# Kernel tuning notes

Hardware: AMD Instinct MI355X
Metric: run time of the kernel (lower is better)

## Reference

```python
import jax, jax.numpy as jnp
import numpy as np

EPS = 0.1        # entropic regularization
MAX_ITER = 50    # fixed iteration count (torch early-stops on host; we run all iters)
P = 1            # cost exponent
N_POINTS = 4096
D_FEAT = 2


def _cost_matrix(x, y):
    # x: [N, D], y: [M, D] -> C: [N, M], sum_d |x_i - y_j|^p
    return jnp.sum(jnp.abs(x[:, None, :] - y[None, :, :]) ** P, axis=-1)


def setup_inputs() -> dict:
    key = jax.random.key(0)
    k1, k2 = jax.random.split(key)
    x = jax.random.normal(k1, (N_POINTS, D_FEAT), dtype=jnp.float32)
    y = jax.random.normal(k2, (N_POINTS, D_FEAT), dtype=jnp.float32)
    return {"x": x, "y": y}


def reference(x, y):
    n, m = x.shape[0], y.shape[0]
    C = _cost_matrix(x, y)  # [N, M]
    log_mu = jnp.log(jnp.full((n,), 1.0 / n, dtype=x.dtype) + 1e-8)
    log_nu = jnp.log(jnp.full((m,), 1.0 / m, dtype=y.dtype) + 1e-8)

    def M(u, v):
        # modified cost: (-C + u_i + v_j) / eps
        return (-C + u[:, None] + v[None, :]) / EPS

    def step(carry, _):
        u, v = carry
        u = EPS * (log_mu - jax.scipy.special.logsumexp(M(u, v), axis=-1)) + u
        v = EPS * (log_nu - jax.scipy.special.logsumexp(M(u, v), axis=-2)) + v
        return (u, v), None

    u0 = jnp.zeros((n,), dtype=x.dtype)
    v0 = jnp.zeros((m,), dtype=y.dtype)
    (u, v), _ = jax.lax.scan(step, (u0, v0), None, length=MAX_ITER)

    pi = jnp.exp(M(u, v))                 # transport plan [N, M]
    cost = jnp.sum(pi * C)                # scalar (reduction='none', 2D input)
    return cost ** (1.0 / P), pi, C
```

## Files before the change

### kernel.cpp

```cpp
#include <hip/hip_runtime.h>


#define NPTS    4096
#define EPS_F   0.1f
#define S_L2E   14.426950408889634f
#define INV_SL  0.0693147180559945f
#define A_LOGMU (-0.8317725207f)
#define N_ITER  50
#define NLEAF   16
#define BSTRIDE 64
#define BAR_INTS ((NLEAF + 1 + NLEAF) * BSTRIDE)

typedef float f4u __attribute__((ext_vector_type(4), aligned(4)));

__device__ __forceinline__ float fexp2(float x) {
#if __has_builtin(__builtin_amdgcn_exp2f)
  return __builtin_amdgcn_exp2f(x);
#else
  float r;
  asm("v_exp_f32 %0, %1" : "=v"(r) : "v"(x));
  return r;
#endif
}

__device__ __forceinline__ float coh_load(const float* p) {
  return __hip_atomic_load(p, __ATOMIC_RELAXED, __HIP_MEMORY_SCOPE_AGENT);
}
__device__ __forceinline__ void coh_store(float* p, float x) {
  __hip_atomic_store(p, x, __ATOMIC_RELAXED, __HIP_MEMORY_SCOPE_AGENT);
}

__device__ __forceinline__ float wave_sum64(float x) {
#pragma unroll
  for (int off = 32; off > 0; off >>= 1) x += __shfl_xor(x, off, 64);
  return x;
}

__device__ __forceinline__ void grid_barrier(int* bar, int k, int arrpl) {
  __syncthreads();
  if (threadIdx.x == 0) {
    const int myleaf = blockIdx.x & (NLEAF - 1);
    const int old = __hip_atomic_fetch_add(bar + myleaf * BSTRIDE, 1,
                                           __ATOMIC_RELAXED,
                                           __HIP_MEMORY_SCOPE_AGENT);
    if (old == arrpl * k - 1)
      __hip_atomic_store(bar + (NLEAF + 1 + myleaf) * BSTRIDE, k,
                         __ATOMIC_RELAXED, __HIP_MEMORY_SCOPE_AGENT);
    for (;;) {
      int mn = k;
#pragma unroll
      for (int rr = 0; rr < NLEAF; ++rr) {
        const int f = __hip_atomic_load(bar + (NLEAF + 1 + rr) * BSTRIDE,
                                        __ATOMIC_RELAXED,
                                        __HIP_MEMORY_SCOPE_AGENT);
        mn = min(mn, f);
      }
      if (mn >= k) break;
      __builtin_amdgcn_s_sleep(1);
    }
  }
  __syncthreads();
}

#define SBLK  512
#define STPB  1024
#define SARR  (SBLK / NLEAF)
#define SCOLS 2048

__device__ __forceinline__ void stage_half(
    const float* __restrict__ part, const float* __restrict__ colp,
    float* __restrict__ sW, float* __restrict__ sC0, float* __restrict__ sC1,
    int tid, int colbase, bool zero) {
  const int c2 = tid * 2;
  const int g = colbase + c2;
  const float4 a = ((const float4*)colp)[g >> 1];
  float w0 = 0.f, w1 = 0.f;
  if (!zero) {
    const float p00 = coh_load(part + g), p01 = coh_load(part + g + 1);
    const float p10 = coh_load(part + NPTS + g);
    const float p11 = coh_load(part + NPTS + g + 1);
    w0 = (A_LOGMU - EPS_F * __logf(p00 + p10)) * S_L2E;
    w1 = (A_LOGMU - EPS_F * __logf(p01 + p11)) * S_L2E;
  }
  float2 W, C0, C1;
  W.x = w0;            W.y = w1;
  C0.x = a.x * S_L2E;  C0.y = a.z * S_L2E;
  C1.x = a.y * S_L2E;  C1.y = a.w * S_L2E;
  *(float2*)(sW + c2)  = W;
  *(float2*)(sC0 + c2) = C0;
  *(float2*)(sC1 + c2) = C1;
  __syncthreads();
}

__device__ __forceinline__ void phase_half(
    const float rx, const float ry, const float* __restrict__ sW,
    const float* __restrict__ sC0, const float* __restrict__ sC1,
    float* __restrict__ pout, int half, int row, int lane) {
  float acc = 0.f;
#pragma unroll
  for (int jt = 0; jt < 8; ++jt) {
    const int j = lane * 4 + jt * 256;
    const float4 W  = *(const float4*)(sW + j);
    const float4 C0 = *(const float4*)(sC0 + j);
    const float4 C1 = *(const float4*)(sC1 + j);
    const float a0 = (W.x - fabsf(rx - C0.x)) - fabsf(ry - C1.x);
    const float a1 = (W.y - fabsf(rx - C0.y)) - fabsf(ry - C1.y);
    const float a2 = (W.z - fabsf(rx - C0.z)) - fabsf(ry - C1.z);
    const float a3 = (W.w - fabsf(rx - C0.w)) - fabsf(ry - C1.w);
    acc += (fexp2(a0) + fexp2(a1)) + (fexp2(a2) + fexp2(a3));
  }
  const float S = wave_sum64(acc);
  if (lane == 0) coh_store(pout + half * NPTS + row, S);
}

__global__ void __launch_bounds__(STPB, 8)
sinkhorn_split(const float* __restrict__ x, const float* __restrict__ y,
               float* __restrict__ pu, float* __restrict__ pv,
               float* __restrict__ out, int* __restrict__ bar) {
  __shared__ float sW[SCOLS], sC0[SCOLS], sC1[SCOLS];
  __shared__ float sCost[16];

  const int tid  = threadIdx.x;
  const int wv   = tid >> 6;
  const int lane = tid & 63;
  const int half = blockIdx.x & 1;
  const int colbase = half * SCOLS;
  const int row  = (blockIdx.x >> 1) * 16 + wv;

  const float2 xr = ((const float2*)x)[row];
  const float2 yr = ((const float2*)y)[row];
  const float rxu = xr.x * S_L2E, ryu = xr.y * S_L2E;
  const float rxv = yr.x * S_L2E, ryv = yr.y * S_L2E;

  int k = 0;
  for (int it = 0; it < N_ITER; ++it) {
    stage_half(pv, y, sW, sC0, sC1, tid, colbase, it == 0);
    phase_half(rxu, ryu, sW, sC0, sC1, pu, half, row, lane);
    grid_barrier(bar, ++k, SARR);
    stage_half(pu, x, sW, sC0, sC1, tid, colbase, false);
    phase_half(rxv, ryv, sW, sC0, sC1, pv, half, row, lane);
    grid_barrier(bar, ++k, SARR);
  }
  stage_half(pv, y, sW, sC0, sC1, tid, colbase, false);

  float* __restrict__ pi = out + 1;
  float* __restrict__ cm = out + 1 + (size_t)NPTS * NPTS;
  const float su = coh_load(pu + row) + coh_load(pu + NPTS + row);
  const float uu = (A_LOGMU - EPS_F * __logf(su)) * S_L2E;

  float costacc = 0.f;
#pragma unroll 2
  for (int jt = 0; jt < 8; ++jt) {
    const int j = lane * 4 + jt * 256;
    const float4 W  = *(const float4*)(sW + j);
    const float4 C0 = *(const float4*)(sC0 + j);
    const float4 C1 = *(const float4*)(sC1 + j);
    const float s0 = fabsf(rxu - C0.x) + fabsf(ryu - C1.x);
    const float s1 = fabsf(rxu - C0.y) + fabsf(ryu - C1.y);
    const float s2 = fabsf(rxu - C0.z) + fabsf(ryu - C1.z);
    const float s3 = fabsf(rxu - C0.w) + fabsf(ryu - C1.w);
    const float p0 = fexp2((uu + W.x) - s0);
    const float p1 = fexp2((uu + W.y) - s1);
    const float p2 = fexp2((uu + W.z) - s2);
    const float p3 = fexp2((uu + W.w) - s3);
    costacc = fmaf(p0, s0, costacc);
    costacc = fmaf(p1, s1, costacc);
    costacc = fmaf(p2, s2, costacc);
    costacc = fmaf(p3, s3, costacc);
    const size_t off = (size_t)row * NPTS + colbase + j;
    f4u pvv; pvv.x = p0; pvv.y = p1; pvv.z = p2; pvv.w = p3;
    f4u cv;  cv.x = s0 * INV_SL; cv.y = s1 * INV_SL;
    cv.z = s2 * INV_SL; cv.w = s3 * INV_SL;
    *(f4u*)(pi + off) = pvv;
    *(f4u*)(cm + off) = cv;
  }
  const float cw = wave_sum64(costacc);
  if (lane == 0) sCost[wv] = cw;
  __syncthreads();
  if (tid == 0) {
    float c = 0.f;
#pragma unroll
    for (int w = 0; w < 16; ++w) c += sCost[w];
    atomicAdd(out, c * INV_SL);
  }
}

#define FBLK  256
#define FTPB  1024
#define WPB   (FTPB / 64)
#define RPW   2
#define HALFC 2048
#define NJT   (HALFC / 256)
#define FARR  (FBLK / NLEAF)

__device__ __forceinline__ void stageW(const float* __restrict__ win,
                                       float* __restrict__ sW, int tid) {
  const int c = tid * 4;
  const float w0 = coh_load(win + c + 0), w1 = coh_load(win + c + 1);
  const float w2 = coh_load(win + c + 2), w3 = coh_load(win + c + 3);
  float4 W;
  W.x = w0 * S_L2E;  W.y = w1 * S_L2E;  W.z = w2 * S_L2E;  W.w = w3 * S_L2E;
  *(float4*)(sW + c) = W;
  __syncthreads();
}

__device__ __forceinline__ void stageCoords(const float* __restrict__ colp,
                                            float* __restrict__ sC0,
                                            float* __restrict__ sC1, int tid) {
  const int c = tid * 4;
  const float4 a = ((const float4*)colp)[(c >> 1) + 0];
  const float4 b = ((const float4*)colp)[(c >> 1) + 1];
  float4 C0, C1;
  C0.x = a.x * S_L2E; C0.y = a.z * S_L2E; C0.z = b.x * S_L2E; C0.w = b.z * S_L2E;
  C1.x = a.y * S_L2E; C1.y = a.w * S_L2E; C1.z = b.y * S_L2E; C1.w = b.w * S_L2E;
  *(float4*)(sC0 + c) = C0;
  *(float4*)(sC1 + c) = C1;
}

__device__ __forceinline__ void fb_phaseU(const float* __restrict__ sW,
                                          const float (&Dreg)[NJT][RPW][4],
                                          float (*sPart)[RPW],
                                          float* __restrict__ wout,
                                          int row0blk, int wv, int lane,
                                          int tid, int base) {
  float acc0 = 0.f, acc1 = 0.f;
#pragma unroll
  for (int jt = 0; jt < NJT; ++jt) {
    const int j = base + jt * 256;
    const float4 W = *(const float4*)(sW + j);
    acc0 += (fexp2(W.x - Dreg[jt][0][0]) + fexp2(W.y - Dreg[jt][0][1])) +
            (fexp2(W.z - Dreg[jt][0][2]) + fexp2(W.w - Dreg[jt][0][3]));
    acc1 += (fexp2(W.x - Dreg[jt][1][0]) + fexp2(W.y - Dreg[jt][1][1])) +
            (fexp2(W.z - Dreg[jt][1][2]) + fexp2(W.w - Dreg[jt][1][3]));
  }
  const float S0 = wave_sum64(acc0);
  const float S1 = wave_sum64(acc1);
  if (lane == 0) { sPart[wv][0] = S0; sPart[wv][1] = S1; }
  __syncthreads();
  if (tid < 16) {
    const int p = tid >> 1, r = tid & 1;
    const float S = sPart[2 * p][r] + sPart[2 * p + 1][r];
    coh_store(wout + row0blk + p * RPW + r, A_LOGMU - EPS_F * __logf(S));
  }
}

__device__ __forceinline__ void fb_phaseV(const float* __restrict__ rx,
                                          const float* __restrict__ ry,
                                          const float* __restrict__ sW,
                                          const float* __restrict__ sC0,
                                          const float* __restrict__ sC1,
                                          float (*sPart)[RPW],
                                          float* __restrict__ wout,
                                          int row0blk, int wv, int lane,
                                          int tid, int base) {
  float acc0 = 0.f, acc1 = 0.f;
#pragma unroll
  for (int jt = 0; jt < NJT; ++jt) {
    const int j = base + jt * 256;
    const float4 W  = *(const float4*)(sW + j);
    const float4 C0 = *(const float4*)(sC0 + j);
    const float4 C1 = *(const float4*)(sC1 + j);
    {
      const float a0 = (W.x - fabsf(rx[0] - C0.x)) - fabsf(ry[0] - C1.x);
      const float a1 = (W.y - fabsf(rx[0] - C0.y)) - fabsf(ry[0] - C1.y);
      const float a2 = (W.z - fabsf(rx[0] - C0.z)) - fabsf(ry[0] - C1.z);
      const float a3 = (W.w - fabsf(rx[0] - C0.w)) - fabsf(ry[0] - C1.w);
      acc0 += (fexp2(a0) + fexp2(a1)) + (fexp2(a2) + fexp2(a3));
    }
    {
      const float a0 = (W.x - fabsf(rx[1] - C0.x)) - fabsf(ry[1] - C1.x);
      const float a1 = (W.y - fabsf(rx[1] - C0.y)) - fabsf(ry[1] - C1.y);
      const float a2 = (W.z - fabsf(rx[1] - C0.z)) - fabsf(ry[1] - C1.z);
      const float a3 = (W.w - fabsf(rx[1] - C0.w)) - fabsf(ry[1] - C1.w);
      acc1 += (fexp2(a0) + fexp2(a1)) + (fexp2(a2) + fexp2(a3));
    }
  }
  const float S0 = wave_sum64(acc0);
  const float S1 = wave_sum64(acc1);
  if (lane == 0) { sPart[wv][0] = S0; sPart[wv][1] = S1; }
  __syncthreads();
  if (tid < 16) {
    const int p = tid >> 1, r = tid & 1;
    const float S = sPart[2 * p][r] + sPart[2 * p + 1][r];
    coh_store(wout + row0blk + p * RPW + r, A_LOGMU - EPS_F * __logf(S));
  }
}

__global__ void __launch_bounds__(FTPB, 4)
sinkhorn_fallback(const float* __restrict__ x, const float* __restrict__ y,
                  float* __restrict__ u, float* __restrict__ v,
                  float* __restrict__ out, int* __restrict__ bar) {
  __shared__ float sW[NPTS];
  __shared__ float sC0y[NPTS], sC1y[NPTS];
  __shared__ float sC0x[NPTS], sC1x[NPTS];
  __shared__ float sPart[WPB][RPW];
  __shared__ float sCost[WPB];

  const int tid  = threadIdx.x;
  const int wv   = tid >> 6;
  const int lane = tid & 63;
  const int row0blk = blockIdx.x * (WPB / 2) * RPW;
  const int row0 = row0blk + (wv >> 1) * RPW;
  const int base = (wv & 1) * HALFC + lane * 4;

  float rxu[RPW], ryu[RPW], rxv[RPW], ryv[RPW];
#pragma unroll
  for (int r = 0; r < RPW; ++r) {
    const float2 xr = ((const float2*)x)[row0 + r];
    const float2 yr = ((const float2*)y)[row0 + r];
    rxu[r] = xr.x * S_L2E;  ryu[r] = xr.y * S_L2E;
    rxv[r] = yr.x * S_L2E;  ryv[r] = yr.y * S_L2E;
  }

  stageCoords(y, sC0y, sC1y, tid);
  stageCoords(x, sC0x, sC1x, tid);
  __syncthreads();

  float Dreg[NJT][RPW][4];
#pragma unroll
  for (int jt = 0; jt < NJT; ++jt) {
    const int j = base + jt * 256;
    const float4 C0 = *(const float4*)(sC0y + j);
    const float4 C1 = *(const float4*)(sC1y + j);
#pragma unroll
    for (int r = 0; r < RPW; ++r) {
      Dreg[jt][r][0] = fabsf(rxu[r] - C0.x) + fabsf(ryu[r] - C1.x);
      Dreg[jt][r][1] = fabsf(rxu[r] - C0.y) + fabsf(ryu[r] - C1.y);
      Dreg[jt][r][2] = fabsf(rxu[r] - C0.z) + fabsf(ryu[r] - C1.z);
      Dreg[jt][r][3] = fabsf(rxu[r] - C0.w) + fabsf(ryu[r] - C1.w);
    }
  }

  int k = 0;
  for (int it = 0; it < N_ITER; ++it) {
    stageW(v, sW, tid);
    fb_phaseU(sW, Dreg, sPart, u, row0blk, wv, lane, tid, base);
    grid_barrier(bar, ++k, FARR);
    stageW(u, sW, tid);
    fb_phaseV(rxv, ryv, sW, sC0x, sC1x, sPart, v, row0blk, wv, lane, tid, base);
    grid_barrier(bar, ++k, FARR);
  }
  stageW(v, sW, tid);

  float* __restrict__ pi = out + 1;
  float* __restrict__ cm = out + 1 + (size_t)NPTS * NPTS;
  float uu[RPW];
#pragma unroll
  for (int r = 0; r < RPW; ++r) uu[r] = coh_load(u + row0 + r) * S_L2E;

  float costacc = 0.f;
#pragma unroll
  for (int jt = 0; jt < NJT; ++jt) {
    const int j = base + jt * 256;
    const float4 W = *(const float4*)(sW + j);
#pragma unroll
    for (int r = 0; r < RPW; ++r) {
      const float s0 = Dreg[jt][r][0];
      const float s1 = Dreg[jt][r][1];
      const float s2 = Dreg[jt][r][2];
      const float s3 = Dreg[jt][r][3];
      const float p0 = fexp2((uu[r] + W.x) - s0);
      const float p1 = fexp2((uu[r] + W.y) - s1);
      const float p2 = fexp2((uu[r] + W.z) - s2);
      const float p3 = fexp2((uu[r] + W.w) - s3);
      costacc = fmaf(p0, s0, costacc);
      costacc = fmaf(p1, s1, costacc);
      costacc = fmaf(p2, s2, costacc);
      costacc = fmaf(p3, s3, costacc);
      const size_t off = (size_t)(row0 + r) * NPTS + j;
      f4u pvv; pvv.x = p0; pvv.y = p1; pvv.z = p2; pvv.w = p3;
      f4u cv;  cv.x = s0 * INV_SL; cv.y = s1 * INV_SL;
      cv.z = s2 * INV_SL; cv.w = s3 * INV_SL;
      *(f4u*)(pi + off) = pvv;
      *(f4u*)(cm + off) = cv;
    }
  }
  const float cw = wave_sum64(costacc);
  if (lane == 0) sCost[wv] = cw;
  __syncthreads();
  if (tid == 0) {
    float c = 0.f;
#pragma unroll
    for (int w = 0; w < WPB; ++w) c += sCost[w];
    atomicAdd(out, c * INV_SL);
  }
}

__global__ void sinkhorn_init(float* __restrict__ buf, int* __restrict__ bar,
                              float* __restrict__ out) {
  const int i = blockIdx.x * blockDim.x + threadIdx.x;
  if (i < 4 * NPTS) coh_store(buf + i, 0.f);
  if (i < BAR_INTS)
    __hip_atomic_store(bar + i, 0, __ATOMIC_RELAXED, __HIP_MEMORY_SCOPE_AGENT);
  if (i == 0) out[0] = 0.f;
}

extern "C" void kernel_launch(void* const* d_in, const int* in_sizes, int n_in,
                              void* d_out, int out_size, void* d_ws,
                              size_t ws_size, hipStream_t stream) {
  const float* x = (const float*)d_in[0];
  const float* y = (const float*)d_in[1];
  float* pu = (float*)d_ws;
  float* pv = pu + 2 * NPTS;
  int* bar = (int*)(pv + 2 * NPTS);
  float* out = (float*)d_out;

  sinkhorn_init<<<dim3(64), dim3(256), 0, stream>>>(pu, bar, out);

  int maxb = 0;
  hipOccupancyMaxActiveBlocksPerMultiprocessor(&maxb, sinkhorn_split, STPB, 0);

  if (maxb >= 2) {
    void* args[6];
    args[0] = (void*)&x;  args[1] = (void*)&y;
    args[2] = (void*)&pu; args[3] = (void*)&pv;
    args[4] = (void*)&out; args[5] = (void*)&bar;
    hipLaunchCooperativeKernel((void*)sinkhorn_split, dim3(SBLK), dim3(STPB),
                               args, 0, stream);
  } else {
    float* u = pu;
    float* v = pv;
    void* args[6];
    args[0] = (void*)&x;  args[1] = (void*)&y;
    args[2] = (void*)&u;  args[3] = (void*)&v;
    args[4] = (void*)&out; args[5] = (void*)&bar;
    hipLaunchCooperativeKernel((void*)sinkhorn_fallback, dim3(FBLK),
                               dim3(FTPB), args, 0, stream);
  }
}
```

Baseline: 695.4 us.

## Split columns into quarters with two rows per wave and preloaded coordinates

The main cooperative kernel now splits the columns into four quarters instead of two, and each wave handles two rows. Each LDS load of weights and coordinates therefore serves two rows. Both x and y coordinates are staged into shared memory once before the loop, so each iteration only restages the weight vector. Partial sums grow to four per row, which adds global loads to the staging step, and the fallback path is simplified to recompute distances instead of caching them in registers.

```diff
diff --git a/kernel.cpp b/kernel.cpp
--- a/kernel.cpp
+++ b/kernel.cpp
@@ -62,117 +62,147 @@
   __syncthreads();
 }
 
-#define SBLK  512
-#define STPB  1024
-#define SARR  (SBLK / NLEAF)
-#define SCOLS 2048
-
-__device__ __forceinline__ void stage_half(
-    const float* __restrict__ part, const float* __restrict__ colp,
-    float* __restrict__ sW, float* __restrict__ sC0, float* __restrict__ sC1,
-    int tid, int colbase, bool zero) {
-  const int c2 = tid * 2;
-  const int g = colbase + c2;
-  const float4 a = ((const float4*)colp)[g >> 1];
-  float w0 = 0.f, w1 = 0.f;
+#define QBLK  512
+#define QTPB  1024
+#define QARR  (QBLK / NLEAF)
+#define QC    1024
+
+__device__ __forceinline__ void stageWq(const float* __restrict__ part,
+                                        float* __restrict__ sW, int tid,
+                                        int colbase, bool zero) {
+  float w = 0.f;
   if (!zero) {
-    const float p00 = coh_load(part + g), p01 = coh_load(part + g + 1);
-    const float p10 = coh_load(part + NPTS + g);
-    const float p11 = coh_load(part + NPTS + g + 1);
-    w0 = (A_LOGMU - EPS_F * __logf(p00 + p10)) * S_L2E;
-    w1 = (A_LOGMU - EPS_F * __logf(p01 + p11)) * S_L2E;
-  }
-  float2 W, C0, C1;
-  W.x = w0;            W.y = w1;
-  C0.x = a.x * S_L2E;  C0.y = a.z * S_L2E;
-  C1.x = a.y * S_L2E;  C1.y = a.w * S_L2E;
-  *(float2*)(sW + c2)  = W;
-  *(float2*)(sC0 + c2) = C0;
-  *(float2*)(sC1 + c2) = C1;
-  __syncthreads();
-}
-
-__device__ __forceinline__ void phase_half(
-    const float rx, const float ry, const float* __restrict__ sW,
-    const float* __restrict__ sC0, const float* __restrict__ sC1,
-    float* __restrict__ pout, int half, int row, int lane) {
-  float acc = 0.f;
-#pragma unroll
-  for (int jt = 0; jt < 8; ++jt) {
+    const int g = colbase + tid;
+    const float s = ((coh_load(part + g) + coh_load(part + NPTS + g)) +
+                     coh_load(part + 2 * NPTS + g)) +
+                    coh_load(part + 3 * NPTS + g);
+    w = (A_LOGMU - INV_SL * __log2f(s)) * S_L2E;
+  }
+  sW[tid] = w;
+  __syncthreads();
+}
+
+__device__ __forceinline__ void phaseq(
+    const float rx0, const float ry0, const float rx1, const float ry1,
+    const float* __restrict__ sW, const float* __restrict__ sC0,
+    const float* __restrict__ sC1, float* __restrict__ pout, int q, int row0,
+    int lane) {
+  float acc0 = 0.f, acc1 = 0.f;
+#pragma unroll
+  for (int jt = 0; jt < 4; ++jt) {
     const int j = lane * 4 + jt * 256;
     const float4 W  = *(const float4*)(sW + j);
     const float4 C0 = *(const float4*)(sC0 + j);
     const float4 C1 = *(const float4*)(sC1 + j);
-    const float a0 = (W.x - fabsf(rx - C0.x)) - fabsf(ry - C1.x);
-    const float a1 = (W.y - fabsf(rx - C0.y)) - fabsf(ry - C1.y);
-    const float a2 = (W.z - fabsf(rx - C0.z)) - fabsf(ry - C1.z);
-    const float a3 = (W.w - fabsf(rx - C0.w)) - fabsf(ry - C1.w);
-    acc += (fexp2(a0) + fexp2(a1)) + (fexp2(a2) + fexp2(a3));
-  }
-  const float S = wave_sum64(acc);
-  if (lane == 0) coh_store(pout + half * NPTS + row, S);
-}
-
-__global__ void __launch_bounds__(STPB, 8)
-sinkhorn_split(const float* __restrict__ x, const float* __restrict__ y,
-               float* __restrict__ pu, float* __restrict__ pv,
-               float* __restrict__ out, int* __restrict__ bar) {
-  __shared__ float sW[SCOLS], sC0[SCOLS], sC1[SCOLS];
+    {
+      const float a0 = (W.x - fabsf(rx0 - C0.x)) - fabsf(ry0 - C1.x);
+      const float a1 = (W.y - fabsf(rx0 - C0.y)) - fabsf(ry0 - C1.y);
+      const float a2 = (W.z - fabsf(rx0 - C0.z)) - fabsf(ry0 - C1.z);
+      const float a3 = (W.w - fabsf(rx0 - C0.w)) - fabsf(ry0 - C1.w);
+      acc0 += (fexp2(a0) + fexp2(a1)) + (fexp2(a2) + fexp2(a3));
+    }
+    {
+      const float a0 = (W.x - fabsf(rx1 - C0.x)) - fabsf(ry1 - C1.x);
+      const float a1 = (W.y - fabsf(rx1 - C0.y)) - fabsf(ry1 - C1.y);
+      const float a2 = (W.z - fabsf(rx1 - C0.z)) - fabsf(ry1 - C1.z);
+      const float a3 = (W.w - fabsf(rx1 - C0.w)) - fabsf(ry1 - C1.w);
+      acc1 += (fexp2(a0) + fexp2(a1)) + (fexp2(a2) + fexp2(a3));
+    }
+  }
+  const float S0 = wave_sum64(acc0);
+  const float S1 = wave_sum64(acc1);
+  if (lane == 0) {
+    coh_store(pout + q * NPTS + row0, S0);
+    coh_store(pout + q * NPTS + row0 + 1, S1);
+  }
+}
+
+__global__ void __launch_bounds__(QTPB, 8)
+sinkhorn_quarter(const float* __restrict__ x, const float* __restrict__ y,
+                 float* __restrict__ pu, float* __restrict__ pv,
+                 float* __restrict__ out, int* __restrict__ bar) {
+  __shared__ float sW[QC];
+  __shared__ float sC0u[QC], sC1u[QC];
+  __shared__ float sC0v[QC], sC1v[QC];
   __shared__ float sCost[16];
 
   const int tid  = threadIdx.x;
   const int wv   = tid >> 6;
   const int lane = tid & 63;
-  const int half = blockIdx.x & 1;
-  const int colbase = half * SCOLS;
-  const int row  = (blockIdx.x >> 1) * 16 + wv;
-
-  const float2 xr = ((const float2*)x)[row];
-  const float2 yr = ((const float2*)y)[row];
-  const float rxu = xr.x * S_L2E, ryu = xr.y * S_L2E;
-  const float rxv = yr.x * S_L2E, ryv = yr.y * S_L2E;
+  const int q    = blockIdx.x & 3;
+  const int rg   = blockIdx.x >> 2;
+  const int row0 = rg * 32 + wv * 2;
+  const int colbase = q * QC;
+
+  float rxu[2], ryu[2], rxv[2], ryv[2];
+#pragma unroll
+  for (int r = 0; r < 2; ++r) {
+    const float2 xr = ((const float2*)x)[row0 + r];
+    const float2 yr = ((const float2*)y)[row0 + r];
+    rxu[r] = xr.x * S_L2E;  ryu[r] = xr.y * S_L2E;
+    rxv[r] = yr.x * S_L2E;  ryv[r] = yr.y * S_L2E;
+  }
+
+  {
+    const int g = colbase + tid;
+    const float2 yc = ((const float2*)y)[g];
+    const float2 xc = ((const float2*)x)[g];
+    sC0u[tid] = yc.x * S_L2E;  sC1u[tid] = yc.y * S_L2E;
+    sC0v[tid] = xc.x * S_L2E;  sC1v[tid] = xc.y * S_L2E;
+  }
+  __syncthreads();
 
   int k = 0;
   for (int it = 0; it < N_ITER; ++it) {
-    stage_half(pv, y, sW, sC0, sC1, tid, colbase, it == 0);
-    phase_half(rxu, ryu, sW, sC0, sC1, pu, half, row, lane);
-    grid_barrier(bar, ++k, SARR);
-    stage_half(pu, x, sW, sC0, sC1, tid, colbase, false);
-    phase_half(rxv, ryv, sW, sC0, sC1, pv, half, row, lane);
-    grid_barrier(bar, ++k, SARR);
-  }
-  stage_half(pv, y, sW, sC0, sC1, tid, colbase, false);
+    stageWq(pv, sW, tid, colbase, it == 0);
+    phaseq(rxu[0], ryu[0], rxu[1], ryu[1], sW, sC0u, sC1u, pu, q, row0, lane);
+    grid_barrier(bar, ++k, QARR);
+    stageWq(pu, sW, tid, colbase, false);
+    phaseq(rxv[0], ryv[0], rxv[1], ryv[1], sW, sC0v, sC1v, pv, q, row0, lane);
+    grid_barrier(bar, ++k, QARR);
+  }
+  stageWq(pv, sW, tid, colbase, false);
 
   float* __restrict__ pi = out + 1;
   float* __restrict__ cm = out + 1 + (size_t)NPTS * NPTS;
-  const float su = coh_load(pu + row) + coh_load(pu + NPTS + row);
-  const float uu = (A_LOGMU - EPS_F * __logf(su)) * S_L2E;
+  float uu[2];
+#pragma unroll
+  for (int r = 0; r < 2; ++r) {
+    const int g = row0 + r;
+    const float su = ((coh_load(pu + g) + coh_load(pu + NPTS + g)) +
+                      coh_load(pu + 2 * NPTS + g)) +
+                     coh_load(pu + 3 * NPTS + g);
+    uu[r] = (A_LOGMU - INV_SL * __log2f(su)) * S_L2E;
+  }
 
   float costacc = 0.f;
-#pragma unroll 2
-  for (int jt = 0; jt < 8; ++jt) {
+#pragma unroll
+  for (int jt = 0; jt < 4; ++jt) {
     const int j = lane * 4 + jt * 256;
     const float4 W  = *(const float4*)(sW + j);
-    const float4 C0 = *(const float4*)(sC0 + j);
-    const float4 C1 = *(const float4*)(sC1 + j);
-    const float s0 = fabsf(rxu - C0.x) + fabsf(ryu - C1.x);
-    const float s1 = fabsf(rxu - C0.y) + fabsf(ryu - C1.y);
-    const float s2 = fabsf(rxu - C0.z) + fabsf(ryu - C1.z);
-    const float s3 = fabsf(rxu - C0.w) + fabsf(ryu - C1.w);
-    const float p0 = fexp2((uu + W.x) - s0);
-    const float p1 = fexp2((uu + W.y) - s1);
-    const float p2 = fexp2((uu + W.z) - s2);
-    const float p3 = fexp2((uu + W.w) - s3);
-    costacc = fmaf(p0, s0, costacc);
-    costacc = fmaf(p1, s1, costacc);
-    costacc = fmaf(p2, s2, costacc);
-    costacc = fmaf(p3, s3, costacc);
-    const size_t off = (size_t)row * NPTS + colbase + j;
-    f4u pvv; pvv.x = p0; pvv.y = p1; pvv.z = p2; pvv.w = p3;
-    f4u cv;  cv.x = s0 * INV_SL; cv.y = s1 * INV_SL;
-    cv.z = s2 * INV_SL; cv.w = s3 * INV_SL;
-    *(f4u*)(pi + off) = pvv;
-    *(f4u*)(cm + off) = cv;
+    const float4 C0 = *(const float4*)(sC0u + j);
+    const float4 C1 = *(const float4*)(sC1u + j);
+#pragma unroll
+    for (int r = 0; r < 2; ++r) {
+      const float s0 = fabsf(rxu[r] - C0.x) + fabsf(ryu[r] - C1.x);
+      const float s1 = fabsf(rxu[r] - C0.y) + fabsf(ryu[r] - C1.y);
+      const float s2 = fabsf(rxu[r] - C0.z) + fabsf(ryu[r] - C1.z);
+      const float s3 = fabsf(rxu[r] - C0.w) + fabsf(ryu[r] - C1.w);
+      const float p0 = fexp2((uu[r] + W.x) - s0);
+      const float p1 = fexp2((uu[r] + W.y) - s1);
+      const float p2 = fexp2((uu[r] + W.z) - s2);
+      const float p3 = fexp2((uu[r] + W.w) - s3);
+      costacc = fmaf(p0, s0, costacc);
+      costacc = fmaf(p1, s1, costacc);
+      costacc = fmaf(p2, s2, costacc);
+      costacc = fmaf(p3, s3, costacc);
+      const size_t off = (size_t)(row0 + r) * NPTS + colbase + j;
+      f4u pvv; pvv.x = p0; pvv.y = p1; pvv.z = p2; pvv.w = p3;
+      f4u cv;  cv.x = s0 * INV_SL; cv.y = s1 * INV_SL;
+      cv.z = s2 * INV_SL; cv.w = s3 * INV_SL;
+      *(f4u*)(pi + off) = pvv;
+      *(f4u*)(cm + off) = cv;
+    }
   }
   const float cw = wave_sum64(costacc);
   if (lane == 0) sCost[wv] = cw;
@@ -193,8 +223,8 @@
 #define NJT   (HALFC / 256)
 #define FARR  (FBLK / NLEAF)
 
-__device__ __forceinline__ void stageW(const float* __restrict__ win,
-                                       float* __restrict__ sW, int tid) {
+__device__ __forceinline__ void fb_stageW(const float* __restrict__ win,
+                                          float* __restrict__ sW, int tid) {
   const int c = tid * 4;
   const float w0 = coh_load(win + c + 0), w1 = coh_load(win + c + 1);
   const float w2 = coh_load(win + c + 2), w3 = coh_load(win + c + 3);
@@ -204,9 +234,10 @@
   __syncthreads();
 }
 
-__device__ __forceinline__ void stageCoords(const float* __restrict__ colp,
-                                            float* __restrict__ sC0,
-                                            float* __restrict__ sC1, int tid) {
+__device__ __forceinline__ void fb_stageCoords(const float* __restrict__ colp,
+                                               float* __restrict__ sC0,
+                                               float* __restrict__ sC1,
+                                               int tid) {
   const int c = tid * 4;
   const float4 a = ((const float4*)colp)[(c >> 1) + 0];
   const float4 b = ((const float4*)colp)[(c >> 1) + 1];
@@ -217,42 +248,15 @@
   *(float4*)(sC1 + c) = C1;
 }
 
-__device__ __forceinline__ void fb_phaseU(const float* __restrict__ sW,
-                                          const float (&Dreg)[NJT][RPW][4],
-                                          float (*sPart)[RPW],
-                                          float* __restrict__ wout,
-                                          int row0blk, int wv, int lane,
-                                          int tid, int base) {
-  float acc0 = 0.f, acc1 = 0.f;
-#pragma unroll
-  for (int jt = 0; jt < NJT; ++jt) {
-    const int j = base + jt * 256;
-    const float4 W = *(const float4*)(sW + j);
-    acc0 += (fexp2(W.x - Dreg[jt][0][0]) + fexp2(W.y - Dreg[jt][0][1])) +
-            (fexp2(W.z - Dreg[jt][0][2]) + fexp2(W.w - Dreg[jt][0][3]));
-    acc1 += (fexp2(W.x - Dreg[jt][1][0]) + fexp2(W.y - Dreg[jt][1][1])) +
-            (fexp2(W.z - Dreg[jt][1][2]) + fexp2(W.w - Dreg[jt][1][3]));
-  }
-  const float S0 = wave_sum64(acc0);
-  const float S1 = wave_sum64(acc1);
-  if (lane == 0) { sPart[wv][0] = S0; sPart[wv][1] = S1; }
-  __syncthreads();
-  if (tid < 16) {
-    const int p = tid >> 1, r = tid & 1;
-    const float S = sPart[2 * p][r] + sPart[2 * p + 1][r];
-    coh_store(wout + row0blk + p * RPW + r, A_LOGMU - EPS_F * __logf(S));
-  }
-}
-
-__device__ __forceinline__ void fb_phaseV(const float* __restrict__ rx,
-                                          const float* __restrict__ ry,
-                                          const float* __restrict__ sW,
-                                          const float* __restrict__ sC0,
-                                          const float* __restrict__ sC1,
-                                          float (*sPart)[RPW],
-                                          float* __restrict__ wout,
-                                          int row0blk, int wv, int lane,
-                                          int tid, int base) {
+__device__ __forceinline__ void fb_phase(const float* __restrict__ rx,
+                                         const float* __restrict__ ry,
+                                         const float* __restrict__ sW,
+                                         const float* __restrict__ sC0,
+                                         const float* __restrict__ sC1,
+                                         float (*sPart)[RPW],
+                                         float* __restrict__ wout,
+                                         int row0blk, int wv, int lane,
+                                         int tid, int base) {
   float acc0 = 0.f, acc1 = 0.f;
 #pragma unroll
   for (int jt = 0; jt < NJT; ++jt) {
@@ -312,35 +316,20 @@
     rxv[r] = yr.x * S_L2E;  ryv[r] = yr.y * S_L2E;
   }
 
-  stageCoords(y, sC0y, sC1y, tid);
-  stageCoords(x, sC0x, sC1x, tid);
-  __syncthreads();
-
-  float Dreg[NJT][RPW][4];
-#pragma unroll
-  for (int jt = 0; jt < NJT; ++jt) {
-    const int j = base + jt * 256;
-    const float4 C0 = *(const float4*)(sC0y + j);
-    const float4 C1 = *(const float4*)(sC1y + j);
-#pragma unroll
-    for (int r = 0; r < RPW; ++r) {
-      Dreg[jt][r][0] = fabsf(rxu[r] - C0.x) + fabsf(ryu[r] - C1.x);
-      Dreg[jt][r][1] = fabsf(rxu[r] - C0.y) + fabsf(ryu[r] - C1.y);
-      Dreg[jt][r][2] = fabsf(rxu[r] - C0.z) + fabsf(ryu[r] - C1.z);
-      Dreg[jt][r][3] = fabsf(rxu[r] - C0.w) + fabsf(ryu[r] - C1.w);
-    }
-  }
+  fb_stageCoords(y, sC0y, sC1y, tid);
+  fb_stageCoords(x, sC0x, sC1x, tid);
+  __syncthreads();
 
   int k = 0;
   for (int it = 0; it < N_ITER; ++it) {
-    stageW(v, sW, tid);
-    fb_phaseU(sW, Dreg, sPart, u, row0blk, wv, lane, tid, base);
+    fb_stageW(v, sW, tid);
+    fb_phase(rxu, ryu, sW, sC0y, sC1y, sPart, u, row0blk, wv, lane, tid, base);
     grid_barrier(bar, ++k, FARR);
-    stageW(u, sW, tid);
-    fb_phaseV(rxv, ryv, sW, sC0x, sC1x, sPart, v, row0blk, wv, lane, tid, base);
+    fb_stageW(u, sW, tid);
+    fb_phase(rxv, ryv, sW, sC0x, sC1x, sPart, v, row0blk, wv, lane, tid, base);
     grid_barrier(bar, ++k, FARR);
   }
-  stageW(v, sW, tid);
+  fb_stageW(v, sW, tid);
 
   float* __restrict__ pi = out + 1;
   float* __restrict__ cm = out + 1 + (size_t)NPTS * NPTS;
@@ -349,16 +338,18 @@
   for (int r = 0; r < RPW; ++r) uu[r] = coh_load(u + row0 + r) * S_L2E;
 
   float costacc = 0.f;
-#pragma unroll
+#pragma unroll 2
   for (int jt = 0; jt < NJT; ++jt) {
     const int j = base + jt * 256;
-    const float4 W = *(const float4*)(sW + j);
+    const float4 W  = *(const float4*)(sW + j);
+    const float4 C0 = *(const float4*)(sC0y + j);
+    const float4 C1 = *(const float4*)(sC1y + j);
 #pragma unroll
     for (int r = 0; r < RPW; ++r) {
-      const float s0 = Dreg[jt][r][0];
-      const float s1 = Dreg[jt][r][1];
-      const float s2 = Dreg[jt][r][2];
-      const float s3 = Dreg[jt][r][3];
+      const float s0 = fabsf(rxu[r] - C0.x) + fabsf(ryu[r] - C1.x);
+      const float s1 = fabsf(rxu[r] - C0.y) + fabsf(ryu[r] - C1.y);
+      const float s2 = fabsf(rxu[r] - C0.z) + fabsf(ryu[r] - C1.z);
+      const float s3 = fabsf(rxu[r] - C0.w) + fabsf(ryu[r] - C1.w);
       const float p0 = fexp2((uu[r] + W.x) - s0);
       const float p1 = fexp2((uu[r] + W.y) - s1);
       const float p2 = fexp2((uu[r] + W.z) - s2);
@@ -389,7 +380,7 @@
 __global__ void sinkhorn_init(float* __restrict__ buf, int* __restrict__ bar,
                               float* __restrict__ out) {
   const int i = blockIdx.x * blockDim.x + threadIdx.x;
-  if (i < 4 * NPTS) coh_store(buf + i, 0.f);
+  if (i < 8 * NPTS) coh_store(buf + i, 0.f);
   if (i < BAR_INTS)
     __hip_atomic_store(bar + i, 0, __ATOMIC_RELAXED, __HIP_MEMORY_SCOPE_AGENT);
   if (i == 0) out[0] = 0.f;
@@ -401,21 +392,22 @@
   const float* x = (const float*)d_in[0];
   const float* y = (const float*)d_in[1];
   float* pu = (float*)d_ws;
-  float* pv = pu + 2 * NPTS;
-  int* bar = (int*)(pv + 2 * NPTS);
+  float* pv = pu + 4 * NPTS;
+  int* bar = (int*)(pv + 4 * NPTS);
   float* out = (float*)d_out;
 
-  sinkhorn_init<<<dim3(64), dim3(256), 0, stream>>>(pu, bar, out);
+  sinkhorn_init<<<dim3(128), dim3(256), 0, stream>>>(pu, bar, out);
 
   int maxb = 0;
-  hipOccupancyMaxActiveBlocksPerMultiprocessor(&maxb, sinkhorn_split, STPB, 0);
+  hipOccupancyMaxActiveBlocksPerMultiprocessor(&maxb, sinkhorn_quarter, QTPB,
+                                               0);
 
   if (maxb >= 2) {
     void* args[6];
     args[0] = (void*)&x;  args[1] = (void*)&y;
     args[2] = (void*)&pu; args[3] = (void*)&pv;
     args[4] = (void*)&out; args[5] = (void*)&bar;
-    hipLaunchCooperativeKernel((void*)sinkhorn_split, dim3(SBLK), dim3(STPB),
+    hipLaunchCooperativeKernel((void*)sinkhorn_quarter, dim3(QBLK), dim3(QTPB),
                                args, 0, stream);
   } else {
     float* u = pu;
```

After: 716.4 us. +3.0%, slower.
